# Performance work log

Measured on AMD Instinct MI355X. Metric: run time of the kernel, lower is better.

The kernel has to match this reference:

```python
import jax, jax.numpy as jnp
import numpy as np

D, NH, DH, DM = 1024, 16, 64, 4096
B, S = 2, 2048
EPS = 1e-5


def _layernorm(x, w, b):
    mu = jnp.mean(x, axis=-1, keepdims=True)
    var = jnp.mean((x - mu) ** 2, axis=-1, keepdims=True)
    return (x - mu) * jax.lax.rsqrt(var + EPS) * w + b


def setup_inputs() -> dict:
    key = jax.random.key(0)
    ks = jax.random.split(key, 8)
    scale = D ** (-0.5)
    x = jax.random.normal(ks[0], (B, S, D), dtype=jnp.float32)
    WQ = jax.random.normal(ks[1], (NH, D, DH), dtype=jnp.float32) * scale
    WK = jax.random.normal(ks[2], (NH, D, DH), dtype=jnp.float32) * scale
    WV = jax.random.normal(ks[3], (NH, D, DH), dtype=jnp.float32) * scale
    WO = jax.random.normal(ks[4], (NH, DH, D), dtype=jnp.float32) * scale
    # MLP: torch Linear default init ~ U(-1/sqrt(fan_in), 1/sqrt(fan_in)); stored as [in, out]
    W1 = jax.random.uniform(ks[5], (D, DM), dtype=jnp.float32, minval=-1.0, maxval=1.0) * D ** (-0.5)
    b1 = jnp.zeros((DM,), dtype=jnp.float32)
    W2 = jax.random.uniform(ks[6], (DM, D), dtype=jnp.float32, minval=-1.0, maxval=1.0) * DM ** (-0.5)
    b2 = jnp.zeros((D,), dtype=jnp.float32)
    ln1_w = jnp.ones((D,), dtype=jnp.float32)
    ln1_b = jnp.zeros((D,), dtype=jnp.float32)
    ln2_w = jnp.ones((D,), dtype=jnp.float32)
    ln2_b = jnp.zeros((D,), dtype=jnp.float32)
    return {"x": x, "WQ": WQ, "WK": WK, "WV": WV, "WO": WO,
            "W1": W1, "b1": b1, "W2": W2, "b2": b2,
            "ln1_w": ln1_w, "ln1_b": ln1_b, "ln2_w": ln2_w, "ln2_b": ln2_b}


def reference(x, WQ, WK, WV, WO, W1, b1, W2, b2, ln1_w, ln1_b, ln2_w, ln2_b):
    s = x.shape[1]
    dh = WQ.shape[-1]
    r = x
    h = _layernorm(x, ln1_w, ln1_b)
    # batched across all heads (original loops over h; math identical)
    Q = jnp.einsum('bsd,hde->bhse', h, WQ)
    K = jnp.einsum('bsd,hde->bhse', h, WK)
    V = jnp.einsum('bsd,hde->bhse', h, WV)
    scores = jnp.einsum('bhqe,bhke->bhqk', Q, K) / jnp.sqrt(jnp.float32(dh))
    causal = jnp.tril(jnp.ones((s, s), dtype=bool))  # True = keep
    scores = jnp.where(causal, scores, -jnp.inf)
    attn = jax.nn.softmax(scores, axis=-1)
    ctx = jnp.einsum('bhqk,bhke->bhqe', attn, V)
    ao = jnp.einsum('bhqe,hed->bqd', ctx, WO)  # sum over heads
    x = r + ao
    h2 = _layernorm(x, ln2_w, ln2_b)
    mlp = jax.nn.gelu(h2 @ W1 + b1, approximate=False) @ W2 + b2
    return x + mlp
```

## Files before the change

### kernel.cpp

```cpp
#include <hip/hip_runtime.h>
#include <hip/hip_bf16.h>
#include <cstdint>

#define D_MODEL 1024
#define NHEADS 16
#define DHEAD 64
#define DMLP 4096
#define BATCH 2
#define SEQ 2048
#define ROWS (BATCH*SEQ)
#define LN_EPS 1e-5f

typedef __attribute__((ext_vector_type(8))) short short8;
typedef __attribute__((ext_vector_type(4))) float f32x4;

typedef const __attribute__((address_space(1))) uint32_t* gas_ptr;
typedef __attribute__((address_space(3))) uint32_t* las_ptr;

__device__ __forceinline__ short f2bf(float f) {
  union { float f; uint32_t u; } v; v.f = f;
  uint32_t r = v.u + 0x7FFFu + ((v.u >> 16) & 1u);
  return (short)(r >> 16);
}
__device__ __forceinline__ float bf2f(short s) {
  union { uint32_t u; float f; } v; v.u = ((uint32_t)(uint16_t)s) << 16;
  return v.f;
}

__global__ void ln_kernel(const float* __restrict__ x, const float* __restrict__ w,
                          const float* __restrict__ b, short* __restrict__ out) {
  int row = blockIdx.x;
  int t = threadIdx.x;
  const float4 v = ((const float4*)(x + (size_t)row * D_MODEL))[t];
  float s = v.x + v.y + v.z + v.w;
  float s2 = v.x*v.x + v.y*v.y + v.z*v.z + v.w*v.w;
#pragma unroll
  for (int k = 1; k < 64; k <<= 1) { s += __shfl_xor(s, k); s2 += __shfl_xor(s2, k); }
  __shared__ float red[8];
  int wv = t >> 6;
  if ((t & 63) == 0) { red[wv] = s; red[wv + 4] = s2; }
  __syncthreads();
  s = red[0] + red[1] + red[2] + red[3];
  s2 = red[4] + red[5] + red[6] + red[7];
  float mu = s * (1.0f / D_MODEL);
  float var = s2 * (1.0f / D_MODEL) - mu * mu;
  float rstd = rsqrtf(var + LN_EPS);
  const float4 wv4 = ((const float4*)w)[t];
  const float4 bv4 = ((const float4*)b)[t];
  short4 o4;
  o4.x = f2bf((v.x - mu) * rstd * wv4.x + bv4.x);
  o4.y = f2bf((v.y - mu) * rstd * wv4.y + bv4.y);
  o4.z = f2bf((v.z - mu) * rstd * wv4.z + bv4.z);
  o4.w = f2bf((v.w - mu) * rstd * wv4.w + bv4.w);
  *(short4*)(out + (size_t)row * D_MODEL + t * 4) = o4;
}

__global__ __launch_bounds__(256) void transpose_tile(const float* __restrict__ src, short* __restrict__ dst,
                                                      int R, int C, int srcMatStride) {
  __shared__ float tile[64][65];
  const int m = blockIdx.z;
  const int r0 = blockIdx.y * 64, c0 = blockIdx.x * 64;
  const int tx = threadIdx.x & 15, ty = threadIdx.x >> 4;
  const float* s = src + (size_t)m * srcMatStride + (size_t)r0 * C + c0;
#pragma unroll
  for (int i = 0; i < 4; i++) {
    float4 v = *(const float4*)(s + (size_t)(ty + i * 16) * C + tx * 4);
    tile[ty + i * 16][tx * 4 + 0] = v.x;
    tile[ty + i * 16][tx * 4 + 1] = v.y;
    tile[ty + i * 16][tx * 4 + 2] = v.z;
    tile[ty + i * 16][tx * 4 + 3] = v.w;
  }
  __syncthreads();
  short* d = dst + (size_t)m * C * R + (size_t)c0 * R + r0;
#pragma unroll
  for (int p = 0; p < 4; p++) {
    int c = ty + p * 16;
    int r4 = tx * 4;
    short4 o;
    o.x = f2bf(tile[r4 + 0][c]);
    o.y = f2bf(tile[r4 + 1][c]);
    o.z = f2bf(tile[r4 + 2][c]);
    o.w = f2bf(tile[r4 + 3][c]);
    *(short4*)(d + (size_t)c * R + r4) = o;
  }
}

template<int EPI>
__global__ __launch_bounds__(256) void gemm_bt(const short* __restrict__ A, const short* __restrict__ BT,
    const float* __restrict__ bias, const float* __restrict__ resid,
    float* __restrict__ outf, short* __restrict__ outb, float* __restrict__ part,
    int M, int N, int K, int LDA, int LDB) {
  __shared__ alignas(16) short As[3][4096];
  __shared__ alignas(16) short Bs[3][4096];
  const int t = threadIdx.x;
  const int l = t & 63, w = t >> 6;
  const int l15 = l & 15, l4 = l >> 4;

  const int nx = gridDim.x;
  const int sw = nx >> 3;
  int d = blockIdx.y * nx + blockIdx.x;
  const int xcd = d & 7, li = d >> 3;
  const int bx = xcd * sw + (li % sw);
  const int by = li / sw;
  const int row0 = by * 128, col0 = bx * 128;

  if (EPI == 5) {
    A  += (size_t)blockIdx.z * K;
    BT += (size_t)blockIdx.z * K;
  }
  f32x4 acc[4][4] = {};

  const int gr = w * 16 + (l >> 2);
  const int c8 = ((l & 3) ^ ((l >> 3) & 3)) * 8;
  const short* Ab0 = A  + (size_t)(row0 + gr) * LDA + c8;
  const short* Ab1 = A  + (size_t)(row0 + 64 + gr) * LDA + c8;
  const short* Bb0 = BT + (size_t)(col0 + gr) * LDB + c8;
  const short* Bb1 = BT + (size_t)(col0 + 64 + gr) * LDB + c8;
  char* AsB = (char*)As;
  char* BsB = (char*)Bs;
  const int soff = w * 1024 + l * 16;

  auto stg = [&](int ti) {
    const int bo = (ti % 3) * 8192;
    const int k0 = ti << 5;
    __builtin_amdgcn_global_load_lds((gas_ptr)(Ab0 + k0), (las_ptr)(AsB + bo + soff),        16, 0, 0);
    __builtin_amdgcn_global_load_lds((gas_ptr)(Ab1 + k0), (las_ptr)(AsB + bo + 4096 + soff), 16, 0, 0);
    __builtin_amdgcn_global_load_lds((gas_ptr)(Bb0 + k0), (las_ptr)(BsB + bo + soff),        16, 0, 0);
    __builtin_amdgcn_global_load_lds((gas_ptr)(Bb1 + k0), (las_ptr)(BsB + bo + 4096 + soff), 16, 0, 0);
  };

  const int nk = K >> 5;
  stg(0);
  if (nk > 1) stg(1);
  asm volatile("s_waitcnt vmcnt(4)" ::: "memory");
  __builtin_amdgcn_s_barrier();

  const int wr = (w >> 1) * 64, wc = (w & 1) * 64;
  const int rch = (l4 ^ ((l15 >> 1) & 3)) * 16;
  const char* Arow = AsB + (wr >> 6) * 4096 + l15 * 64 + rch;
  const char* Brow = BsB + (wc >> 6) * 4096 + l15 * 64 + rch;

  for (int ti = 0; ti < nk; ti++) {
    const int bo = (ti % 3) * 8192;
    if (ti + 2 < nk) stg(ti + 2);
    short8 a[4], bfr[4];
#pragma unroll
    for (int m = 0; m < 4; m++) a[m]   = *(const short8*)(Arow + bo + m * 1024);
#pragma unroll
    for (int n = 0; n < 4; n++) bfr[n] = *(const short8*)(Brow + bo + n * 1024);
#pragma unroll
    for (int m = 0; m < 4; m++)
#pragma unroll
      for (int n = 0; n < 4; n++)
        acc[m][n] = __builtin_amdgcn_mfma_f32_16x16x32_bf16(a[m], bfr[n], acc[m][n], 0, 0, 0);
    if (ti + 2 < nk)      { asm volatile("s_waitcnt vmcnt(4)" ::: "memory"); }
    else if (ti + 1 < nk) { asm volatile("s_waitcnt vmcnt(0)" ::: "memory"); }
    __builtin_amdgcn_s_barrier();
  }

#pragma unroll
  for (int m = 0; m < 4; m++) {
#pragma unroll
    for (int n = 0; n < 4; n++) {
#pragma unroll
      for (int j = 0; j < 4; j++) {
        int R_ = row0 + wr + m * 16 + l4 * 4 + j;
        int C_ = col0 + wc + n * 16 + l15;
        float v = acc[m][n][j];
        size_t o = (size_t)R_ * N + C_;
        if (EPI == 0) {
          outb[o] = f2bf(v);
        } else if (EPI == 2) {
          float xx = v + bias[C_];
          outb[o] = f2bf(0.5f * xx * (1.0f + erff(xx * 0.70710678118f)));
        } else if (EPI == 5) {
          if (blockIdx.z == 0) outf[o] = v + (bias ? bias[C_] : 0.0f) + resid[o];
          else part[o] = v;
        }
      }
    }
  }
}

__global__ void reduce1(float* __restrict__ out, const float* __restrict__ p, int n4) {
  for (int i = blockIdx.x * 256 + threadIdx.x; i < n4; i += gridDim.x * 256) {
    float4 o = ((float4*)out)[i];
    float4 q = ((const float4*)p)[i];
    o.x += q.x; o.y += q.y; o.z += q.z; o.w += q.w;
    ((float4*)out)[i] = o;
  }
}

__device__ __forceinline__ void attn_step(
    int kt_, int qt, int bufP,
    const short* __restrict__ base, const short* __restrict__ vbase,
    short8& vWA, short8& vWB,
    short8& vLA, short8& vLB,
    const short8 qf[2],
    char* KsB, char* VtB, char* PlB,
    f32x4 acc[4], float mrun[4], float lrun[4],
    int w, int l, int q0, int vr, int vd0)
{
  const int l15 = l & 15, l4 = l >> 4;
  const int bufQ = bufP ^ 1;
  if (kt_ < qt) {
#pragma unroll
    for (int i = 0; i < 8; i++) {
      int d = vd0 + i;
      int cs = (vr >> 2) ^ ((d >> 3) & 7);
      uint32_t val = (uint32_t)(uint16_t)vWA[i] | ((uint32_t)(uint16_t)vWB[i] << 16);
      *(uint32_t*)(VtB + bufQ * 9216 + d * 144 + cs * 16 + (vr & 3) * 4) = val;
    }
#pragma unroll
    for (int i = 0; i < 2; i++) {
      int g = (w * 2 + i) * 64 + l;
      int key = g >> 3, ck = g & 7;
      const short* src = base + (size_t)((kt_ + 1) * 64 + key) * 3072 + 1024 + ((ck ^ (key & 7)) * 8);
      __builtin_amdgcn_global_load_lds((gas_ptr)src, (las_ptr)(KsB + bufQ * 8192 + g * 16), 16, 0, 0);
    }
  }
  if (kt_ + 2 <= qt) {
    vLA = *(const short8*)(vbase + (size_t)((kt_ + 2) * 64 + 2 * vr) * 3072);
    vLB = *(const short8*)(vbase + (size_t)((kt_ + 2) * 64 + 2 * vr + 1) * 3072);
  }

  f32x4 sc[4];
#pragma unroll
  for (int cb = 0; cb < 4; cb++) {
    f32x4 s = {};
    int key = cb * 16 + l15;
#pragma unroll
    for (int c = 0; c < 2; c++) {
      int ck = (c * 4 + l4) ^ (key & 7);
      short8 kf = *(const short8*)(KsB + bufP * 8192 + key * 128 + ck * 16);
      s = __builtin_amdgcn_mfma_f32_16x16x32_bf16(qf[c], kf, s, 0, 0, 0);
    }
    sc[cb] = s;
  }

  const bool lastt = (kt_ == qt);
  float alpha[4];
#pragma unroll
  for (int jj = 0; jj < 4; jj++) {
    int qg = q0 + l4 * 4 + jj;
    float s0 = sc[0][jj] * 0.125f;
    float s1 = sc[1][jj] * 0.125f;
    float s2 = sc[2][jj] * 0.125f;
    float s3 = sc[3][jj] * 0.125f;
    if (lastt) {
      int kg = kt_ * 64 + l15;
      if (kg      > qg) s0 = -1e30f;
      if (kg + 16 > qg) s1 = -1e30f;
      if (kg + 32 > qg) s2 = -1e30f;
      if (kg + 48 > qg) s3 = -1e30f;
    }
    float rm = fmaxf(fmaxf(s0, s1), fmaxf(s2, s3));
    rm = fmaxf(rm, __shfl_xor(rm, 1));
    rm = fmaxf(rm, __shfl_xor(rm, 2));
    rm = fmaxf(rm, __shfl_xor(rm, 4));
    rm = fmaxf(rm, __shfl_xor(rm, 8));
    float nm = fmaxf(mrun[jj], rm);
    float al = __expf(mrun[jj] - nm);
    mrun[jj] = nm;
    float p0 = __expf(s0 - nm), p1 = __expf(s1 - nm);
    float p2 = __expf(s2 - nm), p3 = __expf(s3 - nm);
    float ps = p0 + p1 + p2 + p3;
    ps += __shfl_xor(ps, 1);
    ps += __shfl_xor(ps, 2);
    ps += __shfl_xor(ps, 4);
    ps += __shfl_xor(ps, 8);
    lrun[jj] = lrun[jj] * al + ps;
    alpha[jj] = al;
    short* pr = (short*)(PlB + (l4 * 4 + jj) * 144);
    pr[l15]      = f2bf(p0);
    pr[16 + l15] = f2bf(p1);
    pr[32 + l15] = f2bf(p2);
    pr[48 + l15] = f2bf(p3);
  }
#pragma unroll
  for (int db = 0; db < 4; db++) {
    f32x4 a = acc[db];
    a[0] *= alpha[0]; a[1] *= alpha[1]; a[2] *= alpha[2]; a[3] *= alpha[3];
    acc[db] = a;
  }
#pragma unroll
  for (int kc = 0; kc < 2; kc++) {
    short8 pf = *(const short8*)(PlB + l15 * 144 + kc * 64 + l4 * 16);
#pragma unroll
    for (int db = 0; db < 4; db++) {
      int d = db * 16 + l15;
      int cs = (kc * 4 + l4) ^ ((d >> 3) & 7);
      short8 vf = *(const short8*)(VtB + bufP * 9216 + d * 144 + cs * 16);
      acc[db] = __builtin_amdgcn_mfma_f32_16x16x32_bf16(pf, vf, acc[db], 0, 0, 0);
    }
  }
}

__global__ __launch_bounds__(256) void attn_mfma(const short* __restrict__ qkv, short* __restrict__ ctx) {
  __shared__ alignas(16) short Ks[2 * 64 * 64];
  __shared__ alignas(16) short Vt[2 * 64 * 72];
  __shared__ alignas(16) short Pl[4][16 * 72];
  const int t = threadIdx.x;
  const int l = t & 63;
  const int w = t >> 6;
  const int l15 = l & 15, l4 = l >> 4;
  const int bh = blockIdx.x;
  const int b = bh >> 4, h = bh & 15;
  const int qt = (gridDim.y - 1) - blockIdx.y;
  const int q0 = qt * 64 + w * 16;

  const short* base = qkv + (size_t)b * SEQ * 3072 + h * 64;

  short8 qf[2];
#pragma unroll
  for (int c = 0; c < 2; c++)
    qf[c] = *(const short8*)(base + (size_t)(q0 + l15) * 3072 + c * 32 + l4 * 8);

  const int vr = t >> 3;
  const int vd0 = (t & 7) * 8;
  const short* vbase = base + 2048 + vd0;

  char* KsB = (char*)Ks;
  char* VtB = (char*)Vt;
  char* PlB = (char*)&Pl[w][0];

  short8 va0, vb0, va1, vb1;
  va0 = *(const short8*)(vbase + (size_t)(2 * vr) * 3072);
  vb0 = *(const short8*)(vbase + (size_t)(2 * vr + 1) * 3072);
  if (qt >= 1) {
    va1 = *(const short8*)(vbase + (size_t)(64 + 2 * vr) * 3072);
    vb1 = *(const short8*)(vbase + (size_t)(64 + 2 * vr + 1) * 3072);
  }
#pragma unroll
  for (int i = 0; i < 8; i++) {
    int d = vd0 + i;
    int cs = (vr >> 2) ^ ((d >> 3) & 7);
    uint32_t val = (uint32_t)(uint16_t)va0[i] | ((uint32_t)(uint16_t)vb0[i] << 16);
    *(uint32_t*)(VtB + d * 144 + cs * 16 + (vr & 3) * 4) = val;
  }
#pragma unroll
  for (int i = 0; i < 2; i++) {
    int g = (w * 2 + i) * 64 + l;
    int key = g >> 3, ck = g & 7;
    const short* src = base + (size_t)key * 3072 + 1024 + ((ck ^ (key & 7)) * 8);
    __builtin_amdgcn_global_load_lds((gas_ptr)src, (las_ptr)(KsB + g * 16), 16, 0, 0);
  }
  __syncthreads();

  f32x4 acc[4] = {};
  float mrun[4] = {-1e30f, -1e30f, -1e30f, -1e30f};
  float lrun[4] = {0.f, 0.f, 0.f, 0.f};

  int kt = 0;
  while (true) {
    attn_step(kt, qt, 0, base, vbase, va1, vb1, va0, vb0, qf,
              KsB, VtB, PlB, acc, mrun, lrun, w, l, q0, vr, vd0);
    __syncthreads();
    if (++kt > qt) break;
    attn_step(kt, qt, 1, base, vbase, va0, vb0, va1, vb1, qf,
              KsB, VtB, PlB, acc, mrun, lrun, w, l, q0, vr, vd0);
    __syncthreads();
    if (++kt > qt) break;
  }

  float inv[4];
#pragma unroll
  for (int jj = 0; jj < 4; jj++) inv[jj] = 1.0f / lrun[jj];
  short* obase = ctx + (size_t)(b * SEQ + q0) * D_MODEL + h * 64;
#pragma unroll
  for (int db = 0; db < 4; db++)
#pragma unroll
    for (int jj = 0; jj < 4; jj++)
      obase[(size_t)(l4 * 4 + jj) * D_MODEL + db * 16 + l15] = f2bf(acc[db][jj] * inv[jj]);
}

extern "C" void kernel_launch(void* const* d_in, const int* in_sizes, int n_in,
                              void* d_out, int out_size, void* d_ws, size_t ws_size,
                              hipStream_t stream) {
  (void)in_sizes; (void)n_in; (void)out_size; (void)ws_size;
  const float* x    = (const float*)d_in[0];
  const float* WQ   = (const float*)d_in[1];
  const float* WK   = (const float*)d_in[2];
  const float* WV   = (const float*)d_in[3];
  const float* WO   = (const float*)d_in[4];
  const float* W1   = (const float*)d_in[5];
  const float* b1   = (const float*)d_in[6];
  const float* W2   = (const float*)d_in[7];
  const float* b2   = (const float*)d_in[8];
  const float* ln1w = (const float*)d_in[9];
  const float* ln1b = (const float*)d_in[10];
  const float* ln2w = (const float*)d_in[11];
  const float* ln2b = (const float*)d_in[12];
  float* out = (float*)d_out;

  char* p = (char*)d_ws;
  short* h1    = (short*)p; p += (size_t)ROWS * D_MODEL * 2;
  short* ctx   = (short*)p; p += (size_t)ROWS * D_MODEL * 2;
  short* h2    = (short*)p; p += (size_t)ROWS * D_MODEL * 2;
  short* m1    = (short*)p; p += (size_t)ROWS * DMLP * 2;
  short* wqkvT = (short*)p; p += (size_t)3 * D_MODEL * D_MODEL * 2;
  short* woT   = (short*)p; p += (size_t)D_MODEL * D_MODEL * 2;
  short* w1T   = (short*)p; p += (size_t)D_MODEL * DMLP * 2;
  short* w2T   = (short*)p; p += (size_t)D_MODEL * DMLP * 2;
  short* qkv   = (short*)p; p += (size_t)ROWS * 3 * D_MODEL * 2;

  float* fp1 = (float*)qkv;

  transpose_tile<<<dim3(1, 16, 16), 256, 0, stream>>>(WQ, wqkvT,                   1024, 64, D_MODEL * DHEAD);
  transpose_tile<<<dim3(1, 16, 16), 256, 0, stream>>>(WK, wqkvT + 1024 * 1024,     1024, 64, D_MODEL * DHEAD);
  transpose_tile<<<dim3(1, 16, 16), 256, 0, stream>>>(WV, wqkvT + 2 * 1024 * 1024, 1024, 64, D_MODEL * DHEAD);
  transpose_tile<<<dim3(16, 16, 1), 256, 0, stream>>>(WO, woT, 1024, 1024, 0);
  transpose_tile<<<dim3(64, 16, 1), 256, 0, stream>>>(W1, w1T, 1024, 4096, 0);
  transpose_tile<<<dim3(16, 64, 1), 256, 0, stream>>>(W2, w2T, 4096, 1024, 0);

  ln_kernel<<<ROWS, 256, 0, stream>>>(x, ln1w, ln1b, h1);
  gemm_bt<0><<<dim3(3 * D_MODEL / 128, ROWS / 128), 256, 0, stream>>>(
      h1, wqkvT, nullptr, nullptr, nullptr, qkv, nullptr,
      ROWS, 3 * D_MODEL, D_MODEL, D_MODEL, D_MODEL);
  attn_mfma<<<dim3(BATCH * NHEADS, SEQ / 64), 256, 0, stream>>>(qkv, ctx);
  gemm_bt<5><<<dim3(D_MODEL / 128, ROWS / 128, 2), 256, 0, stream>>>(
      ctx, woT, nullptr, x, out, nullptr, fp1,
      ROWS, D_MODEL, D_MODEL / 2, D_MODEL, D_MODEL);
  reduce1<<<2048, 256, 0, stream>>>(out, fp1, ROWS * D_MODEL / 4);
  ln_kernel<<<ROWS, 256, 0, stream>>>(out, ln2w, ln2b, h2);
  gemm_bt<2><<<dim3(DMLP / 128, ROWS / 128), 256, 0, stream>>>(
      h2, w1T, b1, nullptr, nullptr, m1, nullptr,
      ROWS, DMLP, D_MODEL, D_MODEL, D_MODEL);
  gemm_bt<5><<<dim3(D_MODEL / 128, ROWS / 128, 2), 256, 0, stream>>>(
      m1, w2T, b2, out, out, nullptr, fp1,
      ROWS, D_MODEL, DMLP / 2, DMLP, DMLP);
  reduce1<<<2048, 256, 0, stream>>>(out, fp1, ROWS * D_MODEL / 4);
}
```

Baseline: 314.7 us.

## Load GEMM B operand directly into registers and fuse split-K reduce with LayerNorm

The GEMM no longer stages the B (weight) tile through LDS. Each wave now loads its B fragments from global memory straight into registers with double buffering, while A keeps a two-stage LDS buffer, and the MFMA block runs at raised priority through s_setprio. This cuts LDS footprint and traffic but adds uncoalesced global B loads, a full vmcnt(0) wait every iteration and shallower prefetch. Separately, the split-K partial reduction after the attention output projection is fused with the second LayerNorm into one kernel, saving one launch and one read/write pass over the residual.

```diff
diff --git a/kernel.cpp b/kernel.cpp
--- a/kernel.cpp
+++ b/kernel.cpp
@@ -55,6 +55,38 @@
   *(short4*)(out + (size_t)row * D_MODEL + t * 4) = o4;
 }
 
+__global__ void reduce_ln(float* __restrict__ out, const float* __restrict__ part,
+                          const float* __restrict__ w, const float* __restrict__ b,
+                          short* __restrict__ h2) {
+  int row = blockIdx.x;
+  int t = threadIdx.x;
+  float4 v = ((float4*)(out + (size_t)row * D_MODEL))[t];
+  const float4 q = ((const float4*)(part + (size_t)row * D_MODEL))[t];
+  v.x += q.x; v.y += q.y; v.z += q.z; v.w += q.w;
+  ((float4*)(out + (size_t)row * D_MODEL))[t] = v;
+  float s = v.x + v.y + v.z + v.w;
+  float s2 = v.x*v.x + v.y*v.y + v.z*v.z + v.w*v.w;
+#pragma unroll
+  for (int k = 1; k < 64; k <<= 1) { s += __shfl_xor(s, k); s2 += __shfl_xor(s2, k); }
+  __shared__ float red[8];
+  int wv = t >> 6;
+  if ((t & 63) == 0) { red[wv] = s; red[wv + 4] = s2; }
+  __syncthreads();
+  s = red[0] + red[1] + red[2] + red[3];
+  s2 = red[4] + red[5] + red[6] + red[7];
+  float mu = s * (1.0f / D_MODEL);
+  float var = s2 * (1.0f / D_MODEL) - mu * mu;
+  float rstd = rsqrtf(var + LN_EPS);
+  const float4 wv4 = ((const float4*)w)[t];
+  const float4 bv4 = ((const float4*)b)[t];
+  short4 o4;
+  o4.x = f2bf((v.x - mu) * rstd * wv4.x + bv4.x);
+  o4.y = f2bf((v.y - mu) * rstd * wv4.y + bv4.y);
+  o4.z = f2bf((v.z - mu) * rstd * wv4.z + bv4.z);
+  o4.w = f2bf((v.w - mu) * rstd * wv4.w + bv4.w);
+  *(short4*)(h2 + (size_t)row * D_MODEL + t * 4) = o4;
+}
+
 __global__ __launch_bounds__(256) void transpose_tile(const float* __restrict__ src, short* __restrict__ dst,
                                                       int R, int C, int srcMatStride) {
   __shared__ float tile[64][65];
@@ -90,16 +122,15 @@
     const float* __restrict__ bias, const float* __restrict__ resid,
     float* __restrict__ outf, short* __restrict__ outb, float* __restrict__ part,
     int M, int N, int K, int LDA, int LDB) {
-  __shared__ alignas(16) short As[3][4096];
-  __shared__ alignas(16) short Bs[3][4096];
+  __shared__ alignas(16) short As[2][4096];
   const int t = threadIdx.x;
   const int l = t & 63, w = t >> 6;
   const int l15 = l & 15, l4 = l >> 4;
 
   const int nx = gridDim.x;
   const int sw = nx >> 3;
-  int d = blockIdx.y * nx + blockIdx.x;
-  const int xcd = d & 7, li = d >> 3;
+  int dd = blockIdx.y * nx + blockIdx.x;
+  const int xcd = dd & 7, li = dd >> 3;
   const int bx = xcd * sw + (li % sw);
   const int by = li / sw;
   const int row0 = by * 128, col0 = bx * 128;
@@ -112,50 +143,80 @@
 
   const int gr = w * 16 + (l >> 2);
   const int c8 = ((l & 3) ^ ((l >> 3) & 3)) * 8;
-  const short* Ab0 = A  + (size_t)(row0 + gr) * LDA + c8;
-  const short* Ab1 = A  + (size_t)(row0 + 64 + gr) * LDA + c8;
-  const short* Bb0 = BT + (size_t)(col0 + gr) * LDB + c8;
-  const short* Bb1 = BT + (size_t)(col0 + 64 + gr) * LDB + c8;
+  const short* Ab0 = A + (size_t)(row0 + gr) * LDA + c8;
+  const short* Ab1 = A + (size_t)(row0 + 64 + gr) * LDA + c8;
   char* AsB = (char*)As;
-  char* BsB = (char*)Bs;
   const int soff = w * 1024 + l * 16;
 
-  auto stg = [&](int ti) {
-    const int bo = (ti % 3) * 8192;
-    const int k0 = ti << 5;
-    __builtin_amdgcn_global_load_lds((gas_ptr)(Ab0 + k0), (las_ptr)(AsB + bo + soff),        16, 0, 0);
-    __builtin_amdgcn_global_load_lds((gas_ptr)(Ab1 + k0), (las_ptr)(AsB + bo + 4096 + soff), 16, 0, 0);
-    __builtin_amdgcn_global_load_lds((gas_ptr)(Bb0 + k0), (las_ptr)(BsB + bo + soff),        16, 0, 0);
-    __builtin_amdgcn_global_load_lds((gas_ptr)(Bb1 + k0), (las_ptr)(BsB + bo + 4096 + soff), 16, 0, 0);
-  };
-
-  const int nk = K >> 5;
-  stg(0);
-  if (nk > 1) stg(1);
-  asm volatile("s_waitcnt vmcnt(4)" ::: "memory");
-  __builtin_amdgcn_s_barrier();
-
   const int wr = (w >> 1) * 64, wc = (w & 1) * 64;
+  const short* Bp = BT + (size_t)(col0 + wc + l15) * LDB + l4 * 8;
+  const size_t bstep = (size_t)16 * LDB;
+
   const int rch = (l4 ^ ((l15 >> 1) & 3)) * 16;
   const char* Arow = AsB + (wr >> 6) * 4096 + l15 * 64 + rch;
-  const char* Brow = BsB + (wc >> 6) * 4096 + l15 * 64 + rch;
-
-  for (int ti = 0; ti < nk; ti++) {
-    const int bo = (ti % 3) * 8192;
-    if (ti + 2 < nk) stg(ti + 2);
-    short8 a[4], bfr[4];
-#pragma unroll
-    for (int m = 0; m < 4; m++) a[m]   = *(const short8*)(Arow + bo + m * 1024);
-#pragma unroll
-    for (int n = 0; n < 4; n++) bfr[n] = *(const short8*)(Brow + bo + n * 1024);
-#pragma unroll
-    for (int m = 0; m < 4; m++)
-#pragma unroll
-      for (int n = 0; n < 4; n++)
-        acc[m][n] = __builtin_amdgcn_mfma_f32_16x16x32_bf16(a[m], bfr[n], acc[m][n], 0, 0, 0);
-    if (ti + 2 < nk)      { asm volatile("s_waitcnt vmcnt(4)" ::: "memory"); }
-    else if (ti + 1 < nk) { asm volatile("s_waitcnt vmcnt(0)" ::: "memory"); }
-    __builtin_amdgcn_s_barrier();
+
+  short8 bA[4], bB[4];
+  const int nk = K >> 5;
+
+#pragma unroll
+  for (int n = 0; n < 4; n++) bA[n] = *(const short8*)(Bp + n * bstep);
+  __builtin_amdgcn_global_load_lds((gas_ptr)(Ab0), (las_ptr)(AsB + soff),        16, 0, 0);
+  __builtin_amdgcn_global_load_lds((gas_ptr)(Ab1), (las_ptr)(AsB + 4096 + soff), 16, 0, 0);
+  asm volatile("s_waitcnt vmcnt(0)" ::: "memory");
+  __builtin_amdgcn_s_barrier();
+
+  int ti = 0;
+  while (true) {
+    {
+      if (ti + 1 < nk) {
+        const short* Bn = Bp + (ti + 1) * 32;
+#pragma unroll
+        for (int n = 0; n < 4; n++) bB[n] = *(const short8*)(Bn + n * bstep);
+        const int k0 = (ti + 1) << 5;
+        __builtin_amdgcn_global_load_lds((gas_ptr)(Ab0 + k0), (las_ptr)(AsB + 8192 + soff),        16, 0, 0);
+        __builtin_amdgcn_global_load_lds((gas_ptr)(Ab1 + k0), (las_ptr)(AsB + 8192 + 4096 + soff), 16, 0, 0);
+      }
+      short8 a[4];
+#pragma unroll
+      for (int m = 0; m < 4; m++) a[m] = *(const short8*)(Arow + m * 1024);
+      __builtin_amdgcn_s_setprio(1);
+#pragma unroll
+      for (int m = 0; m < 4; m++)
+#pragma unroll
+        for (int n = 0; n < 4; n++)
+          acc[m][n] = __builtin_amdgcn_mfma_f32_16x16x32_bf16(a[m], bA[n], acc[m][n], 0, 0, 0);
+      __builtin_amdgcn_s_setprio(0);
+      if (ti + 1 < nk) {
+        asm volatile("s_waitcnt vmcnt(0)" ::: "memory");
+        __builtin_amdgcn_s_barrier();
+      }
+    }
+    if (++ti >= nk) break;
+    {
+      if (ti + 1 < nk) {
+        const short* Bn = Bp + (ti + 1) * 32;
+#pragma unroll
+        for (int n = 0; n < 4; n++) bA[n] = *(const short8*)(Bn + n * bstep);
+        const int k0 = (ti + 1) << 5;
+        __builtin_amdgcn_global_load_lds((gas_ptr)(Ab0 + k0), (las_ptr)(AsB + soff),        16, 0, 0);
+        __builtin_amdgcn_global_load_lds((gas_ptr)(Ab1 + k0), (las_ptr)(AsB + 4096 + soff), 16, 0, 0);
+      }
+      short8 a[4];
+#pragma unroll
+      for (int m = 0; m < 4; m++) a[m] = *(const short8*)(Arow + 8192 + m * 1024);
+      __builtin_amdgcn_s_setprio(1);
+#pragma unroll
+      for (int m = 0; m < 4; m++)
+#pragma unroll
+        for (int n = 0; n < 4; n++)
+          acc[m][n] = __builtin_amdgcn_mfma_f32_16x16x32_bf16(a[m], bB[n], acc[m][n], 0, 0, 0);
+      __builtin_amdgcn_s_setprio(0);
+      if (ti + 1 < nk) {
+        asm volatile("s_waitcnt vmcnt(0)" ::: "memory");
+        __builtin_amdgcn_s_barrier();
+      }
+    }
+    if (++ti >= nk) break;
   }
 
 #pragma unroll
@@ -421,8 +482,7 @@
   gemm_bt<5><<<dim3(D_MODEL / 128, ROWS / 128, 2), 256, 0, stream>>>(
       ctx, woT, nullptr, x, out, nullptr, fp1,
       ROWS, D_MODEL, D_MODEL / 2, D_MODEL, D_MODEL);
-  reduce1<<<2048, 256, 0, stream>>>(out, fp1, ROWS * D_MODEL / 4);
-  ln_kernel<<<ROWS, 256, 0, stream>>>(out, ln2w, ln2b, h2);
+  reduce_ln<<<ROWS, 256, 0, stream>>>(out, fp1, ln2w, ln2b, h2);
   gemm_bt<2><<<dim3(DMLP / 128, ROWS / 128), 256, 0, stream>>>(
       h2, w1T, b1, nullptr, nullptr, m1, nullptr,
       ROWS, DMLP, D_MODEL, D_MODEL, D_MODEL);
```

Result: slower. 398.0 us (+26.5%).
